# Kernel optimization log

Measured on AMD Instinct MI355X. Metric: run time of the kernel, lower is better.

## Reference

```python
import jax, jax.numpy as jnp
import numpy as np

T = 500      # max_context_length (hard-coded in the original module)
D = 8192     # feature width of h / rows of c2q, q2c


def setup_inputs() -> dict:
    key = jax.random.key(0)
    k1, k2, k3 = jax.random.split(key, 3)
    h = jax.random.normal(k1, (1, T, D), dtype=jnp.float32)
    c2q = jax.random.normal(k2, (D, T), dtype=jnp.float32)
    q2c = jax.random.normal(k3, (D, T), dtype=jnp.float32)
    return {"h": h, "c2q": c2q, "q2c": q2c}


def reference(h, c2q, q2c):
    # Original loop builds, for each context position c:
    #   beta_c = concat([h[0,c], c2q.T[c], h[0,c]*c2q.T[c], h[0,c]*q2c.T[c]])  # [4D]
    # and stacks then transposes -> G of shape [4D, T].
    H = h[0]        # [T, D]
    C = c2q.T       # [T, D]
    Q = q2c.T       # [T, D]
    G = jnp.concatenate([H, C, H * C, H * Q], axis=1)  # [T, 4D]
    return G.T      # [4D, T]
```

## Files before the change

### kernel.cpp

```cpp
#include <hip/hip_runtime.h>
#include <hip/hip_bf16.h>

#define TCTX 500
#define DFEAT 8192
#define BD 16
#define LDS_S 500

typedef float v4f __attribute__((ext_vector_type(4)));

__global__ __launch_bounds__(512) void MegaMerge_77283641524594_kernel(
    const float* __restrict__ h,
    const float* __restrict__ c2q,
    const float* __restrict__ q2c,
    float* __restrict__ out)
{
    __shared__ float hs[BD * LDS_S];

    const int tid = threadIdx.x;
    const int d0  = blockIdx.x * BD;

    const int t4   = tid & 127;
    const int rowg = tid >> 7;
    const bool act = (t4 < 125);

    v4f cpre[4], qpre[4];
    if (act) {
        #pragma unroll
        for (int k = 0; k < 4; ++k) {
            const size_t j = (size_t)(d0 + rowg + 4 * k);
            cpre[k] = *reinterpret_cast<const v4f*>(&c2q[j * TCTX + t4 * 4]);
            qpre[k] = *reinterpret_cast<const v4f*>(&q2c[j * TCTX + t4 * 4]);
        }
    }

    {
        const int dc = (tid & 3) * 4;
        const int tr = tid >> 2;
        #pragma unroll
        for (int p = 0; p < 4; ++p) {
            const int t = p * 128 + tr;
            if (t < TCTX) {
                const v4f v = *reinterpret_cast<const v4f*>(
                    &h[(size_t)t * DFEAT + d0 + dc]);
                hs[(dc + 0) * LDS_S + t] = v.x;
                hs[(dc + 1) * LDS_S + t] = v.y;
                hs[(dc + 2) * LDS_S + t] = v.z;
                hs[(dc + 3) * LDS_S + t] = v.w;
            }
        }
    }
    __syncthreads();

    if (act) {
        const size_t sec = (size_t)DFEAT * TCTX;
        #pragma unroll
        for (int k = 0; k < 4; ++k) {
            const int dl = rowg + 4 * k;
            const size_t j = (size_t)(d0 + dl);
            const v4f hv = *reinterpret_cast<const v4f*>(
                &hs[dl * LDS_S + t4 * 4]);
            const v4f c = cpre[k];
            const v4f q = qpre[k];
            const v4f hc = hv * c;
            const v4f hq = hv * q;
            const size_t o = j * TCTX + t4 * 4;
            __builtin_nontemporal_store(hv, reinterpret_cast<v4f*>(&out[o          ]));
            __builtin_nontemporal_store(c,  reinterpret_cast<v4f*>(&out[o + sec    ]));
            __builtin_nontemporal_store(hc, reinterpret_cast<v4f*>(&out[o + 2 * sec]));
            __builtin_nontemporal_store(hq, reinterpret_cast<v4f*>(&out[o + 3 * sec]));
        }
    }
}

extern "C" void kernel_launch(void* const* d_in, const int* in_sizes, int n_in,
                              void* d_out, int out_size, void* d_ws, size_t ws_size,
                              hipStream_t stream) {
    const float* h   = (const float*)d_in[0];
    const float* c2q = (const float*)d_in[1];
    const float* q2c = (const float*)d_in[2];
    float* out = (float*)d_out;

    dim3 grid(DFEAT / BD);
    dim3 block(512);
    MegaMerge_77283641524594_kernel<<<grid, block, 0, stream>>>(h, c2q, q2c, out);
}
```

Measured before the change: 28.13 us.

## Tile the context dimension across a 2D grid and use regular stores

```diff
diff --git a/kernel.cpp b/kernel.cpp
--- a/kernel.cpp
+++ b/kernel.cpp
@@ -4,11 +4,12 @@
 #define TCTX 500
 #define DFEAT 8192
 #define BD 16
-#define LDS_S 500
+#define TT 128
+#define LDS_S (TT + 4)
 
 typedef float v4f __attribute__((ext_vector_type(4)));
 
-__global__ __launch_bounds__(512) void MegaMerge_77283641524594_kernel(
+__global__ __launch_bounds__(256) void MegaMerge_77283641524594_kernel(
     const float* __restrict__ h,
     const float* __restrict__ c2q,
     const float* __restrict__ q2c,
@@ -18,18 +19,20 @@
 
     const int tid = threadIdx.x;
     const int d0  = blockIdx.x * BD;
+    const int t0  = blockIdx.y * TT;
 
-    const int t4   = tid & 127;
-    const int rowg = tid >> 7;
-    const bool act = (t4 < 125);
+    const int t4   = tid & 31;
+    const int rowg = tid >> 5;
+    const int t    = t0 + t4 * 4;
+    const bool act = (t < TCTX);
 
-    v4f cpre[4], qpre[4];
+    v4f cpre[2], qpre[2];
     if (act) {
         #pragma unroll
-        for (int k = 0; k < 4; ++k) {
-            const size_t j = (size_t)(d0 + rowg + 4 * k);
-            cpre[k] = *reinterpret_cast<const v4f*>(&c2q[j * TCTX + t4 * 4]);
-            qpre[k] = *reinterpret_cast<const v4f*>(&q2c[j * TCTX + t4 * 4]);
+        for (int k = 0; k < 2; ++k) {
+            const size_t j = (size_t)(d0 + rowg * 2 + k);
+            cpre[k] = *reinterpret_cast<const v4f*>(&c2q[j * TCTX + t]);
+            qpre[k] = *reinterpret_cast<const v4f*>(&q2c[j * TCTX + t]);
         }
     }
 
@@ -37,15 +40,16 @@
         const int dc = (tid & 3) * 4;
         const int tr = tid >> 2;
         #pragma unroll
-        for (int p = 0; p < 4; ++p) {
-            const int t = p * 128 + tr;
-            if (t < TCTX) {
+        for (int p = 0; p < 2; ++p) {
+            const int tl = p * 64 + tr;
+            const int tg = t0 + tl;
+            if (tg < TCTX) {
                 const v4f v = *reinterpret_cast<const v4f*>(
-                    &h[(size_t)t * DFEAT + d0 + dc]);
-                hs[(dc + 0) * LDS_S + t] = v.x;
-                hs[(dc + 1) * LDS_S + t] = v.y;
-                hs[(dc + 2) * LDS_S + t] = v.z;
-                hs[(dc + 3) * LDS_S + t] = v.w;
+                    &h[(size_t)tg * DFEAT + d0 + dc]);
+                hs[(dc + 0) * LDS_S + tl] = v.x;
+                hs[(dc + 1) * LDS_S + tl] = v.y;
+                hs[(dc + 2) * LDS_S + tl] = v.z;
+                hs[(dc + 3) * LDS_S + tl] = v.w;
             }
         }
     }
@@ -54,8 +58,8 @@
     if (act) {
         const size_t sec = (size_t)DFEAT * TCTX;
         #pragma unroll
-        for (int k = 0; k < 4; ++k) {
-            const int dl = rowg + 4 * k;
+        for (int k = 0; k < 2; ++k) {
+            const int dl = rowg * 2 + k;
             const size_t j = (size_t)(d0 + dl);
             const v4f hv = *reinterpret_cast<const v4f*>(
                 &hs[dl * LDS_S + t4 * 4]);
@@ -63,11 +67,11 @@
             const v4f q = qpre[k];
             const v4f hc = hv * c;
             const v4f hq = hv * q;
-            const size_t o = j * TCTX + t4 * 4;
-            __builtin_nontemporal_store(hv, reinterpret_cast<v4f*>(&out[o          ]));
-            __builtin_nontemporal_store(c,  reinterpret_cast<v4f*>(&out[o + sec    ]));
-            __builtin_nontemporal_store(hc, reinterpret_cast<v4f*>(&out[o + 2 * sec]));
-            __builtin_nontemporal_store(hq, reinterpret_cast<v4f*>(&out[o + 3 * sec]));
+            const size_t o = j * TCTX + t;
+            *reinterpret_cast<v4f*>(&out[o          ]) = hv;
+            *reinterpret_cast<v4f*>(&out[o + sec    ]) = c;
+            *reinterpret_cast<v4f*>(&out[o + 2 * sec]) = hc;
+            *reinterpret_cast<v4f*>(&out[o + 3 * sec]) = hq;
         }
     }
 }
@@ -80,7 +84,7 @@
     const float* q2c = (const float*)d_in[2];
     float* out = (float*)d_out;
 
-    dim3 grid(DFEAT / BD);
-    dim3 block(512);
+    dim3 grid(DFEAT / BD, (TCTX + TT - 1) / TT);
+    dim3 block(256);
     MegaMerge_77283641524594_kernel<<<grid, block, 0, stream>>>(h, c2q, q2c, out);
 }
```

New measurement: 26.74 us. 1.05x faster.
